# Optimization experiments

Measured on AMD Instinct MI355X. Metric: run time of the kernel, lower is better.

## Reference

```python
import jax, jax.numpy as jnp
import numpy as np

N_NODES = 100000
N_EDGES = 1600000
IN_C = 128
OUT_C = 64
NEG_SLOPE = 0.2  # PyG GATConv default
EPS = 1e-16      # PyG softmax denominator guard


def setup_inputs() -> dict:
    key = jax.random.key(0)
    k1, k2, k3, k4, k5, k6 = jax.random.split(key, 6)
    x = jax.random.normal(k1, (N_NODES, IN_C), dtype=jnp.float32)
    edge_index = jax.random.randint(k2, (2, N_EDGES), 0, N_NODES, dtype=jnp.int64)
    # Learned params (GATConv with heads=1): linear weight, attention vectors, bias
    W = jax.random.normal(k3, (IN_C, OUT_C), dtype=jnp.float32) * (1.0 / np.sqrt(IN_C))
    a_src = jax.random.normal(k4, (OUT_C,), dtype=jnp.float32) * (1.0 / np.sqrt(OUT_C))
    a_dst = jax.random.normal(k5, (OUT_C,), dtype=jnp.float32) * (1.0 / np.sqrt(OUT_C))
    b = jax.random.normal(k6, (OUT_C,), dtype=jnp.float32) * 0.01
    return {"x": x, "edge_index": edge_index, "W": W, "a_src": a_src, "a_dst": a_dst, "b": b}


def reference(x, edge_index, W, a_src, a_dst, b):
    N = x.shape[0]
    h = x @ W  # [N, OUT_C] transformed node features
    # add self loops (PyG default add_self_loops=True)
    loops = jnp.arange(N, dtype=edge_index.dtype)
    src = jnp.concatenate([edge_index[0], loops])  # [E+N]
    dst = jnp.concatenate([edge_index[1], loops])  # [E+N]
    # attention logits per edge: leaky_relu(a_src . h_src + a_dst . h_dst)
    s_src = h @ a_src  # [N]
    s_dst = h @ a_dst  # [N]
    logits = jax.nn.leaky_relu(s_src[src] + s_dst[dst], NEG_SLOPE)  # [E+N]
    # segment softmax over incoming edges of each destination node
    seg_max = jax.ops.segment_max(logits, dst, num_segments=N)  # [N]
    e = jnp.exp(logits - seg_max[dst])
    denom = jax.ops.segment_sum(e, dst, num_segments=N)  # [N]
    coef = e / (denom[dst] + EPS)  # [E+N]
    # weighted scatter-add of source messages
    out = jax.ops.segment_sum(coef[:, None] * h[src], dst, num_segments=N) + b  # [N, OUT_C]
    return jax.nn.elu(out)
```

## Files before the change

### kernel.cpp

```cpp
#include <hip/hip_runtime.h>
#include <math.h>

#define IN_C 128
#define OUT_C 64
#define NEG_SLOPE 0.2f
#define GAT_EPS 1e-16f

#define CSH 11
#define CN 2048
#define CAPC 36864
#define FSH 6
#define FN 64
#define FPC 32
#define CAPB 1536
#define RND 2048
#define SUBS 16
#define PACKS 20

typedef unsigned int uint;
typedef unsigned short ushort;
typedef __attribute__((ext_vector_type(8))) short bf16x8;
typedef __attribute__((ext_vector_type(4))) float f32x4;

__device__ __forceinline__ ushort f2bf(float f) {
    uint u = __float_as_uint(f);
    return (ushort)((u + 0x7fffu + ((u >> 16) & 1u)) >> 16);
}

__global__ __launch_bounds__(256) void gemm_kernel(
    const float* __restrict__ x, const float* __restrict__ W,
    const float* __restrict__ a_src, const float* __restrict__ a_dst,
    ushort* __restrict__ h16, float* __restrict__ s_src, float* __restrict__ s_dst,
    int N, int* __restrict__ zero_ptr, int zero_n)
{
    __shared__ __align__(16) ushort xs[64 * 128];
    __shared__ __align__(16) ushort Wl[128 * 64];
    const int t = threadIdx.x;

    {
        int zi = blockIdx.x * 256 + t;
        if (zi < zero_n) zero_ptr[zi] = 0;
    }

    #pragma unroll
    for (int q = 0; q < 8; q++) {
        float4 wv = ((const float4*)W)[t * 8 + q];
        #pragma unroll
        for (int e = 0; e < 4; e++) {
            int L = t * 32 + q * 4 + e;
            int k = L >> 6, col = L & 63;
            int kc = k >> 5, kg = (k >> 3) & 3, j = k & 7;
            int ct = col >> 4, c16 = col & 15;
            float v = (e == 0) ? wv.x : (e == 1) ? wv.y : (e == 2) ? wv.z : wv.w;
            Wl[(((kc * 4 + ct) * 4 + kg) * 16 + c16) * 8 + j] = f2bf(v);
        }
    }
    const int row0 = blockIdx.x * 64;
    {
        int row_l = t >> 2;
        int grow = row0 + row_l;
        #pragma unroll
        for (int qq = 0; qq < 4; qq++) {
            int kq = (t & 3) * 4 + qq;
            float4 v0 = make_float4(0.f, 0.f, 0.f, 0.f);
            float4 v1 = v0;
            if (grow < N) {
                const float4* xp = (const float4*)(x + (size_t)grow * IN_C + kq * 8);
                v0 = xp[0]; v1 = xp[1];
            }
            uint4 pk;
            pk.x = (uint)f2bf(v0.x) | ((uint)f2bf(v0.y) << 16);
            pk.y = (uint)f2bf(v0.z) | ((uint)f2bf(v0.w) << 16);
            pk.z = (uint)f2bf(v1.x) | ((uint)f2bf(v1.y) << 16);
            pk.w = (uint)f2bf(v1.z) | ((uint)f2bf(v1.w) << 16);
            int slot = row_l * 16 + (kq ^ (row_l & 7));
            *(uint4*)&xs[slot * 8] = pk;
        }
    }
    __syncthreads();

    const int wv_ = t >> 6;
    const int l = t & 63;
    const int c16 = l & 15;
    const int quad = l >> 4;
    const int row_a = wv_ * 16 + c16;

    f32x4 acc[4] = {{0.f, 0.f, 0.f, 0.f}, {0.f, 0.f, 0.f, 0.f},
                    {0.f, 0.f, 0.f, 0.f}, {0.f, 0.f, 0.f, 0.f}};

    #pragma unroll
    for (int kc = 0; kc < 4; kc++) {
        int kq = kc * 4 + quad;
        bf16x8 a = *(const bf16x8*)&xs[(row_a * 16 + (kq ^ (row_a & 7))) * 8];
        #pragma unroll
        for (int ct = 0; ct < 4; ct++) {
            bf16x8 b = *(const bf16x8*)&Wl[(((kc * 4 + ct) * 4 + quad) * 16 + c16) * 8];
            acc[ct] = __builtin_amdgcn_mfma_f32_16x16x32_bf16(a, b, acc[ct], 0, 0, 0);
        }
    }

    float as4[4], ad4[4];
    #pragma unroll
    for (int ct = 0; ct < 4; ct++) {
        as4[ct] = a_src[ct * 16 + c16];
        ad4[ct] = a_dst[ct * 16 + c16];
    }
    #pragma unroll
    for (int reg = 0; reg < 4; reg++) {
        int row = row0 + wv_ * 16 + quad * 4 + reg;
        float ps = acc[0][reg] * as4[0] + acc[1][reg] * as4[1]
                 + acc[2][reg] * as4[2] + acc[3][reg] * as4[3];
        float pd = acc[0][reg] * ad4[0] + acc[1][reg] * ad4[1]
                 + acc[2][reg] * ad4[2] + acc[3][reg] * ad4[3];
        ps += __shfl_xor(ps, 1);  pd += __shfl_xor(pd, 1);
        ps += __shfl_xor(ps, 2);  pd += __shfl_xor(pd, 2);
        ps += __shfl_xor(ps, 4);  pd += __shfl_xor(pd, 4);
        ps += __shfl_xor(ps, 8);  pd += __shfl_xor(pd, 8);
        if (row < N) {
            #pragma unroll
            for (int ct = 0; ct < 4; ct++)
                h16[(size_t)row * OUT_C + ct * 16 + c16] = f2bf(acc[ct][reg]);
            if (c16 == 0) { s_src[row] = ps; s_dst[row] = pd; }
        }
    }
}

__global__ __launch_bounds__(256) void partA_kernel(
    const int* __restrict__ src, const int* __restrict__ dst,
    int* __restrict__ ccurA, int* __restrict__ ebufA, int E, int NC)
{
    __shared__ int scnt[64], sofs[64], gbase[64], rbase[64];
    __shared__ int rbuf[RND];
    __shared__ int garr[RND];
    const int t = threadIdx.x;
    const int e0 = blockIdx.x * RND;
    int tot = E - e0; if (tot > RND) tot = RND;

    if (t < 64) scnt[t] = 0;
    __syncthreads();
    #pragma unroll
    for (int k = 0; k < RND / 256; k++) {
        int i = k * 256 + t;
        if (i < tot) atomicAdd(&scnt[dst[e0 + i] >> CSH], 1);
    }
    __syncthreads();
    if (t < 64) {
        int v = scnt[t];
        int incl = v;
        #pragma unroll
        for (int off = 1; off < 64; off <<= 1) {
            int u = __shfl_up(incl, off);
            if (t >= off) incl += u;
        }
        int excl = incl - v;
        rbase[t] = excl;
        sofs[t] = excl;
        if (t < NC && v > 0) gbase[t] = t * CAPC + atomicAdd(&ccurA[t], v);
    }
    __syncthreads();
    #pragma unroll
    for (int k = 0; k < RND / 256; k++) {
        int i = k * 256 + t;
        if (i < tot) {
            int d = dst[e0 + i];
            int c = d >> CSH;
            int q = atomicAdd(&sofs[c], 1);
            rbuf[q] = ((d & (CN - 1)) << PACKS) | src[e0 + i];
            int g = gbase[c] + (q - rbase[c]);
            garr[q] = (g < (c + 1) * CAPC) ? g : -1;
        }
    }
    __syncthreads();
    for (int i = t; i < tot; i += 256) {
        int g = garr[i];
        if (g >= 0) ebufA[g] = rbuf[i];
    }
}

__global__ __launch_bounds__(256) void partB_kernel(
    const int* __restrict__ ccurA, int* __restrict__ ccurB,
    const int* __restrict__ ebufA, int* __restrict__ ebufB, int NC)
{
    __shared__ int scnt[FPC], sofs[FPC], gbase[FPC], rbase[FPC];
    __shared__ int rbuf[RND];
    __shared__ int garr[RND];
    const int c = blockIdx.x / SUBS;
    const int sub = blockIdx.x % SUBS;
    if (c >= NC) return;
    const int t = threadIdx.x;
    int len = ccurA[c]; if (len > CAPC) len = CAPC;
    const int beg = c * CAPC;
    const int nrounds = (len + RND - 1) / RND;

    for (int r = sub; r < nrounds; r += SUBS) {
        const int e0 = beg + r * RND;
        int tot = beg + len - e0; if (tot > RND) tot = RND;
        if (t < FPC) scnt[t] = 0;
        __syncthreads();
        #pragma unroll
        for (int k = 0; k < RND / 256; k++) {
            int i = k * 256 + t;
            if (i < tot) atomicAdd(&scnt[(ebufA[e0 + i] >> (PACKS + FSH)) & (FPC - 1)], 1);
        }
        __syncthreads();
        if (t < FPC) {
            int v = scnt[t];
            int incl = v;
            #pragma unroll
            for (int off = 1; off < FPC; off <<= 1) {
                int u = __shfl_up(incl, off);
                if (t >= off) incl += u;
            }
            int excl = incl - v;
            rbase[t] = excl;
            sofs[t] = excl;
            int fg = c * FPC + t;
            if (v > 0) gbase[t] = fg * CAPB + atomicAdd(&ccurB[fg], v);
        }
        __syncthreads();
        #pragma unroll
        for (int k = 0; k < RND / 256; k++) {
            int i = k * 256 + t;
            if (i < tot) {
                int pk = ebufA[e0 + i];
                int f = (pk >> (PACKS + FSH)) & (FPC - 1);
                int q = atomicAdd(&sofs[f], 1);
                rbuf[q] = pk;
                int g = gbase[f] + (q - rbase[f]);
                garr[q] = (g < (c * FPC + f + 1) * CAPB) ? g : -1;
            }
        }
        __syncthreads();
        for (int i = t; i < tot; i += 256) {
            int g = garr[i];
            if (g >= 0) ebufB[g] = rbuf[i];
        }
        __syncthreads();
    }
}

__global__ __launch_bounds__(256) void nodeB_kernel(
    const int* __restrict__ ccurB, const int* __restrict__ ebufB,
    const float* __restrict__ s_src, const float* __restrict__ s_dst,
    const ushort* __restrict__ h16, const float* __restrict__ bias,
    float* __restrict__ out, int N)
{
    __shared__ int   csr_s[CAPB];
    __shared__ float csr_e[CAPB];
    __shared__ int lhist[FN], lofs[FN + 1], lcur[FN];

    const int b = blockIdx.x;
    const int t = threadIdx.x;
    const int node0 = b << FSH;
    const int nn = min(FN, N - node0);
    int cnt = ccurB[b]; if (cnt > CAPB) cnt = CAPB;
    const int base = b * CAPB;

    if (t < FN) lhist[t] = 0;
    __syncthreads();
    for (int i = t; i < cnt; i += 256)
        atomicAdd(&lhist[(ebufB[base + i] >> PACKS) & (FN - 1)], 1);
    __syncthreads();
    if (t < FN) {
        int v = lhist[t];
        int incl = v;
        #pragma unroll
        for (int off = 1; off < FN; off <<= 1) {
            int u = __shfl_up(incl, off);
            if (t >= off) incl += u;
        }
        lofs[t + 1] = incl;
        lcur[t] = incl - v;
        if (t == 0) lofs[0] = 0;
    }
    __syncthreads();
    for (int i = t; i < cnt; i += 256) {
        int pk = ebufB[base + i];
        int ld = (pk >> PACKS) & (FN - 1);
        int sj = pk & ((1 << PACKS) - 1);
        int q = atomicAdd(&lcur[ld], 1);
        float lg = s_src[sj] + s_dst[node0 + ld];
        lg = (lg > 0.f) ? lg : NEG_SLOPE * lg;
        csr_s[q] = sj;
        csr_e[q] = __expf(lg);
    }
    __syncthreads();

    const int w = t >> 6;
    const int l = t & 63;
    const int h2 = l >> 5;
    const int lp = l & 31;
    const float b0 = bias[2 * lp], b1 = bias[2 * lp + 1];

    for (int nl = w; nl < nn; nl += 4) {
        const int node = node0 + nl;
        const int jb = lofs[nl], je = lofs[nl + 1];
        float acc0 = 0.f, acc1 = 0.f, ds = 0.f;
        int j = jb + h2;
        for (; j + 6 < je; j += 8) {
            int s0 = csr_s[j],     s1 = csr_s[j + 2];
            int s2 = csr_s[j + 4], s3 = csr_s[j + 6];
            float e0 = csr_e[j],     e1 = csr_e[j + 2];
            float e2 = csr_e[j + 4], e3 = csr_e[j + 6];
            uint u0 = *(const uint*)&h16[(size_t)s0 * OUT_C + 2 * lp];
            uint u1 = *(const uint*)&h16[(size_t)s1 * OUT_C + 2 * lp];
            uint u2 = *(const uint*)&h16[(size_t)s2 * OUT_C + 2 * lp];
            uint u3 = *(const uint*)&h16[(size_t)s3 * OUT_C + 2 * lp];
            ds += (e0 + e1) + (e2 + e3);
            acc0 += e0 * __uint_as_float(u0 << 16) + e1 * __uint_as_float(u1 << 16)
                  + e2 * __uint_as_float(u2 << 16) + e3 * __uint_as_float(u3 << 16);
            acc1 += e0 * __uint_as_float(u0 & 0xffff0000u) + e1 * __uint_as_float(u1 & 0xffff0000u)
                  + e2 * __uint_as_float(u2 & 0xffff0000u) + e3 * __uint_as_float(u3 & 0xffff0000u);
        }
        for (; j < je; j += 2) {
            int sj = csr_s[j];
            float e = csr_e[j];
            uint u = *(const uint*)&h16[(size_t)sj * OUT_C + 2 * lp];
            ds += e;
            acc0 += e * __uint_as_float(u << 16);
            acc1 += e * __uint_as_float(u & 0xffff0000u);
        }
        acc0 += __shfl_xor(acc0, 32);
        acc1 += __shfl_xor(acc1, 32);
        ds   += __shfl_xor(ds, 32);

        float ls = s_src[node] + s_dst[node];
        ls = (ls > 0.f) ? ls : NEG_SLOPE * ls;
        float es = __expf(ls);
        uint us = *(const uint*)&h16[(size_t)node * OUT_C + 2 * lp];
        acc0 += es * __uint_as_float(us << 16);
        acc1 += es * __uint_as_float(us & 0xffff0000u);
        ds += es;

        float inv = 1.f / (ds + GAT_EPS);
        float v0 = acc0 * inv + b0;
        float v1 = acc1 * inv + b1;
        v0 = (v0 > 0.f) ? v0 : (__expf(v0) - 1.f);
        v1 = (v1 > 0.f) ? v1 : (__expf(v1) - 1.f);
        if (l < 32) *(float2*)&out[(size_t)node * OUT_C + 2 * lp] = make_float2(v0, v1);
    }
}

extern "C" void kernel_launch(void* const* d_in, const int* in_sizes, int n_in,
                              void* d_out, int out_size, void* d_ws, size_t ws_size,
                              hipStream_t stream)
{
    const float* x     = (const float*)d_in[0];
    const int*   ei    = (const int*)d_in[1];
    const float* W     = (const float*)d_in[2];
    const float* a_src = (const float*)d_in[3];
    const float* a_dst = (const float*)d_in[4];
    const float* b     = (const float*)d_in[5];
    float* out = (float*)d_out;

    const int N = in_sizes[0] / IN_C;
    const int E = in_sizes[1] / 2;
    const int NC = (N + CN - 1) >> CSH;
    const int NFB = (N + FN - 1) >> FSH;
    const int NFB_AL = NC * FPC;
    const int nroundsA = (E + RND - 1) / RND;
    const int GB = (N + 63) / 64;
    const int* src = ei;
    const int* dst = ei + E;

    ushort* h16    = (ushort*)d_ws;
    float* s_src_p = (float*)(h16 + (size_t)N * OUT_C);
    float* s_dst_p = s_src_p + N;
    int*   ccurA   = (int*)(s_dst_p + N);
    int*   ccurB   = ccurA + 64;
    int*   ebufB   = ccurB + NFB_AL;
    int*   ebufA   = (int*)d_out;

    gemm_kernel<<<GB, 256, 0, stream>>>(x, W, a_src, a_dst, h16, s_src_p, s_dst_p,
                                        N, ccurA, 64 + NFB_AL);
    partA_kernel<<<nroundsA, 256, 0, stream>>>(src, dst, ccurA, ebufA, E, NC);
    partB_kernel<<<NC * SUBS, 256, 0, stream>>>(ccurA, ccurB, ebufA, ebufB, NC);
    nodeB_kernel<<<NFB, 256, 0, stream>>>(ccurB, ebufB, s_src_p, s_dst_p, h16, b, out, N);
}
```

Measured before the change: 202.7 us.

## Replace two-pass LDS partitioning with single-pass global-atomic binning by destination block

Removes the two-level partition (coarse chunk then fine 64-node bucket) and instead bins each edge directly into its 64-node bucket using one global atomicAdd per edge, with vectorized int4 loads of src/dst. This eliminates one kernel launch and the intermediate ebufA round trip through memory. In exchange it incurs heavy global atomic contention on ~1.5k counters and uncoalesced scattered writes, and the grid sizing assumes E is roughly a multiple of four.

```diff
diff --git a/kernel.cpp b/kernel.cpp
--- a/kernel.cpp
+++ b/kernel.cpp
@@ -6,15 +6,12 @@
 #define NEG_SLOPE 0.2f
 #define GAT_EPS 1e-16f
 
-#define CSH 11
-#define CN 2048
-#define CAPC 36864
 #define FSH 6
 #define FN 64
 #define FPC 32
 #define CAPB 1536
-#define RND 2048
-#define SUBS 16
+#define CN 2048
+#define CSH 11
 #define PACKS 20
 
 typedef unsigned int uint;
@@ -125,117 +122,33 @@
     }
 }
 
-__global__ __launch_bounds__(256) void partA_kernel(
+__global__ __launch_bounds__(256) void bin_kernel(
     const int* __restrict__ src, const int* __restrict__ dst,
-    int* __restrict__ ccurA, int* __restrict__ ebufA, int E, int NC)
-{
-    __shared__ int scnt[64], sofs[64], gbase[64], rbase[64];
-    __shared__ int rbuf[RND];
-    __shared__ int garr[RND];
-    const int t = threadIdx.x;
-    const int e0 = blockIdx.x * RND;
-    int tot = E - e0; if (tot > RND) tot = RND;
-
-    if (t < 64) scnt[t] = 0;
-    __syncthreads();
-    #pragma unroll
-    for (int k = 0; k < RND / 256; k++) {
-        int i = k * 256 + t;
-        if (i < tot) atomicAdd(&scnt[dst[e0 + i] >> CSH], 1);
-    }
-    __syncthreads();
-    if (t < 64) {
-        int v = scnt[t];
-        int incl = v;
-        #pragma unroll
-        for (int off = 1; off < 64; off <<= 1) {
-            int u = __shfl_up(incl, off);
-            if (t >= off) incl += u;
-        }
-        int excl = incl - v;
-        rbase[t] = excl;
-        sofs[t] = excl;
-        if (t < NC && v > 0) gbase[t] = t * CAPC + atomicAdd(&ccurA[t], v);
-    }
-    __syncthreads();
-    #pragma unroll
-    for (int k = 0; k < RND / 256; k++) {
-        int i = k * 256 + t;
-        if (i < tot) {
-            int d = dst[e0 + i];
-            int c = d >> CSH;
-            int q = atomicAdd(&sofs[c], 1);
-            rbuf[q] = ((d & (CN - 1)) << PACKS) | src[e0 + i];
-            int g = gbase[c] + (q - rbase[c]);
-            garr[q] = (g < (c + 1) * CAPC) ? g : -1;
-        }
-    }
-    __syncthreads();
-    for (int i = t; i < tot; i += 256) {
-        int g = garr[i];
-        if (g >= 0) ebufA[g] = rbuf[i];
-    }
-}
-
-__global__ __launch_bounds__(256) void partB_kernel(
-    const int* __restrict__ ccurA, int* __restrict__ ccurB,
-    const int* __restrict__ ebufA, int* __restrict__ ebufB, int NC)
-{
-    __shared__ int scnt[FPC], sofs[FPC], gbase[FPC], rbase[FPC];
-    __shared__ int rbuf[RND];
-    __shared__ int garr[RND];
-    const int c = blockIdx.x / SUBS;
-    const int sub = blockIdx.x % SUBS;
-    if (c >= NC) return;
-    const int t = threadIdx.x;
-    int len = ccurA[c]; if (len > CAPC) len = CAPC;
-    const int beg = c * CAPC;
-    const int nrounds = (len + RND - 1) / RND;
-
-    for (int r = sub; r < nrounds; r += SUBS) {
-        const int e0 = beg + r * RND;
-        int tot = beg + len - e0; if (tot > RND) tot = RND;
-        if (t < FPC) scnt[t] = 0;
-        __syncthreads();
-        #pragma unroll
-        for (int k = 0; k < RND / 256; k++) {
-            int i = k * 256 + t;
-            if (i < tot) atomicAdd(&scnt[(ebufA[e0 + i] >> (PACKS + FSH)) & (FPC - 1)], 1);
-        }
-        __syncthreads();
-        if (t < FPC) {
-            int v = scnt[t];
-            int incl = v;
-            #pragma unroll
-            for (int off = 1; off < FPC; off <<= 1) {
-                int u = __shfl_up(incl, off);
-                if (t >= off) incl += u;
-            }
-            int excl = incl - v;
-            rbase[t] = excl;
-            sofs[t] = excl;
-            int fg = c * FPC + t;
-            if (v > 0) gbase[t] = fg * CAPB + atomicAdd(&ccurB[fg], v);
-        }
-        __syncthreads();
-        #pragma unroll
-        for (int k = 0; k < RND / 256; k++) {
-            int i = k * 256 + t;
-            if (i < tot) {
-                int pk = ebufA[e0 + i];
-                int f = (pk >> (PACKS + FSH)) & (FPC - 1);
-                int q = atomicAdd(&sofs[f], 1);
-                rbuf[q] = pk;
-                int g = gbase[f] + (q - rbase[f]);
-                garr[q] = (g < (c * FPC + f + 1) * CAPB) ? g : -1;
-            }
-        }
-        __syncthreads();
-        for (int i = t; i < tot; i += 256) {
-            int g = garr[i];
-            if (g >= 0) ebufB[g] = rbuf[i];
-        }
-        __syncthreads();
+    int* __restrict__ ccur, int* __restrict__ ebufB, int E)
+{
+    const int base4 = (blockIdx.x * 256 + threadIdx.x) * 4;
+    if (base4 >= E) return;
+    if (base4 + 3 < E) {
+        int4 s = *(const int4*)(src + base4);
+        int4 d = *(const int4*)(dst + base4);
+        int ds_[4] = {d.x, d.y, d.z, d.w};
+        int ss_[4] = {s.x, s.y, s.z, s.w};
+        #pragma unroll
+        for (int k = 0; k < 4; k++) {
+            int dd = ds_[k], ss = ss_[k];
+            int fb = dd >> FSH;
+            int idx = atomicAdd(&ccur[fb], 1);
+            if (idx < CAPB)
+                ebufB[(size_t)fb * CAPB + idx] = ((dd & (FN - 1)) << PACKS) | ss;
+        }
+    } else {
+        for (int i = base4; i < E; i++) {
+            int dd = dst[i], ss = src[i];
+            int fb = dd >> FSH;
+            int idx = atomicAdd(&ccur[fb], 1);
+            if (idx < CAPB)
+                ebufB[(size_t)fb * CAPB + idx] = ((dd & (FN - 1)) << PACKS) | ss;
+        }
     }
 }
 
@@ -355,25 +268,22 @@
 
     const int N = in_sizes[0] / IN_C;
     const int E = in_sizes[1] / 2;
+    const int NFB = (N + FN - 1) >> FSH;
     const int NC = (N + CN - 1) >> CSH;
-    const int NFB = (N + FN - 1) >> FSH;
     const int NFB_AL = NC * FPC;
-    const int nroundsA = (E + RND - 1) / RND;
     const int GB = (N + 63) / 64;
+    const int GBIN = (E / 4 + 255) / 256;
     const int* src = ei;
     const int* dst = ei + E;
 
     ushort* h16    = (ushort*)d_ws;
     float* s_src_p = (float*)(h16 + (size_t)N * OUT_C);
     float* s_dst_p = s_src_p + N;
-    int*   ccurA   = (int*)(s_dst_p + N);
-    int*   ccurB   = ccurA + 64;
-    int*   ebufB   = ccurB + NFB_AL;
-    int*   ebufA   = (int*)d_out;
+    int*   ccur    = (int*)(s_dst_p + N);
+    int*   ebufB   = ccur + NFB_AL;
 
     gemm_kernel<<<GB, 256, 0, stream>>>(x, W, a_src, a_dst, h16, s_src_p, s_dst_p,
-                                        N, ccurA, 64 + NFB_AL);
-    partA_kernel<<<nroundsA, 256, 0, stream>>>(src, dst, ccurA, ebufA, E, NC);
-    partB_kernel<<<NC * SUBS, 256, 0, stream>>>(ccurA, ccurB, ebufA, ebufB, NC);
-    nodeB_kernel<<<NFB, 256, 0, stream>>>(ccurB, ebufB, s_src_p, s_dst_p, h16, b, out, N);
-}
+                                        N, ccur, NFB_AL);
+    bin_kernel<<<GBIN, 256, 0, stream>>>(src, dst, ccur, ebufB, E);
+    nodeB_kernel<<<NFB, 256, 0, stream>>>(ccur, ebufB, s_src_p, s_dst_p, h16, b, out, N);
+}
```

Measured after the change: 403.7 us. 99.2% more time.
